# Performance work log

Hardware: AMD Instinct MI355X
Metric: run time of the kernel (lower is better)

Reference implementation:

```python
import jax, jax.numpy as jnp
import numpy as np

NUM_HEADS = 8
QK_CH = 1024
V_CH = 1024
Q_DIM = 1024
KV_DIM = 1024
EPS = 1e-5


def layernorm(x, w, b):
    mu = jnp.mean(x, axis=-1, keepdims=True)
    var = jnp.mean(jnp.square(x - mu), axis=-1, keepdims=True)
    return (x - mu) * jax.lax.rsqrt(var + EPS) * w + b


def setup_inputs() -> dict:
    key = jax.random.key(0)
    ks = jax.random.split(key, 8)
    B, Q, K = 8, 512, 4096
    s = 0.02
    return {
        "hidden_states": jax.random.normal(ks[0], (B, Q, Q_DIM), jnp.float32),
        "inputs": jax.random.normal(ks[1], (B, K, KV_DIM), jnp.float32),
        "ln1_w": jnp.ones((Q_DIM,), jnp.float32),
        "ln1_b": jnp.zeros((Q_DIM,), jnp.float32),
        "ln2_w": jnp.ones((KV_DIM,), jnp.float32),
        "ln2_b": jnp.zeros((KV_DIM,), jnp.float32),
        "Wq": jax.random.normal(ks[2], (QK_CH, Q_DIM), jnp.float32) * s,
        "bq": jnp.zeros((QK_CH,), jnp.float32),
        "Wk": jax.random.normal(ks[3], (QK_CH, KV_DIM), jnp.float32) * s,
        "bk": jnp.zeros((QK_CH,), jnp.float32),
        "Wv": jax.random.normal(ks[4], (V_CH, KV_DIM), jnp.float32) * s,
        "bv": jnp.zeros((V_CH,), jnp.float32),
    }


def reference(hidden_states, inputs, ln1_w, ln1_b, ln2_w, ln2_b, Wq, bq, Wk, bk, Wv, bv):
    B, Qlen, _ = hidden_states.shape
    Klen = inputs.shape[1]
    H = NUM_HEADS
    dqk = QK_CH // H
    dv = V_CH // H

    h = layernorm(hidden_states, ln1_w, ln1_b)
    x = layernorm(inputs, ln2_w, ln2_b)

    # torch Linear: y = x W^T + b
    q = (h @ Wq.T + bq).reshape(B, Qlen, H, dqk).transpose(0, 2, 1, 3)  # b h q d
    k = (x @ Wk.T + bk).reshape(B, Klen, H, dqk).transpose(0, 2, 1, 3)  # b h k d
    v = (x @ Wv.T + bv).reshape(B, Klen, H, dv).transpose(0, 2, 1, 3)   # b h k d

    scores = jnp.einsum("bhqd,bhkd->bhqk", q, k) / jnp.sqrt(jnp.float32(dqk))
    probs = jax.nn.softmax(scores, axis=-1)
    ctx = jnp.einsum("bhqk,bhkd->bhqd", probs, v)
    ctx = ctx.transpose(0, 2, 1, 3).reshape(B, Qlen, H * dv)

    # use_query_residual=True
    return hidden_states + ctx
```

## Files before the change

kernel.cpp:

```cpp
#include <hip/hip_runtime.h>
#include <hip/hip_fp8.h>

typedef __attribute__((ext_vector_type(8))) short short8;
typedef __attribute__((ext_vector_type(4))) short bf16x4;
typedef __attribute__((ext_vector_type(4))) float f32x4;
typedef __attribute__((ext_vector_type(2))) long i64x2;

#define DEV __device__ __forceinline__

DEV unsigned short f2bf(float f) {
    unsigned int u = __builtin_bit_cast(unsigned int, f);
    u += 0x7fffu + ((u >> 16) & 1u);
    return (unsigned short)(u >> 16);
}

DEV unsigned char f2fp8(float f) {
    return __hip_fp8_e4m3(f).__x;
}

#define GLOAD16(gp, lp)                                                        \
    __builtin_amdgcn_global_load_lds(                                          \
        (const __attribute__((address_space(1))) void*)(gp),                   \
        (__attribute__((address_space(3))) void*)(lp), 16, 0, 0)

__global__ __launch_bounds__(256) void prep(
    const float* __restrict__ hidden, const float* __restrict__ inputs,
    const float* __restrict__ ln1w, const float* __restrict__ ln1b,
    const float* __restrict__ ln2w, const float* __restrict__ ln2b,
    const float* __restrict__ Wq, const float* __restrict__ Wk, const float* __restrict__ Wv,
    unsigned char* __restrict__ LNh8, unsigned char* __restrict__ LNx8,
    unsigned char* __restrict__ Wq8, unsigned char* __restrict__ Wk8, unsigned char* __restrict__ Wv8)
{
    if (blockIdx.x < 9216) {
        int row = blockIdx.x * 4 + (threadIdx.x >> 6);
        int lane = threadIdx.x & 63;
        const float *src, *wp, *bp; unsigned char* dst;
        if (row < 4096) { src = hidden + (size_t)row * 1024; wp = ln1w; bp = ln1b; dst = LNh8 + (size_t)row * 1024; }
        else { int r = row - 4096; src = inputs + (size_t)r * 1024; wp = ln2w; bp = ln2b; dst = LNx8 + (size_t)r * 1024; }

        f32x4 v[4];
        float s = 0.f, ss = 0.f;
#pragma unroll
        for (int i = 0; i < 4; ++i) {
            v[i] = *reinterpret_cast<const f32x4*>(src + lane * 16 + i * 4);
#pragma unroll
            for (int j = 0; j < 4; ++j) { s += v[i][j]; ss += v[i][j] * v[i][j]; }
        }
#pragma unroll
        for (int off = 32; off >= 1; off >>= 1) { s += __shfl_xor(s, off); ss += __shfl_xor(ss, off); }
        float mu = s * (1.f / 1024.f);
        float var = fmaxf(ss * (1.f / 1024.f) - mu * mu, 0.f);
        float rs = rsqrtf(var + 1e-5f);

        unsigned char by[16];
#pragma unroll
        for (int i = 0; i < 4; ++i) {
            f32x4 wv = *reinterpret_cast<const f32x4*>(wp + lane * 16 + i * 4);
            f32x4 bv = *reinterpret_cast<const f32x4*>(bp + lane * 16 + i * 4);
#pragma unroll
            for (int j = 0; j < 4; ++j)
                by[i * 4 + j] = f2fp8((v[i][j] - mu) * rs * wv[j] + bv[j]);
        }
        int o = (lane * 16) & 63;
        int s0 = (o < 32) ? 2 * o : 2 * (o - 32) + 8;
        unsigned char* base = dst + (lane >> 2) * 64;
        *reinterpret_cast<unsigned long long*>(base + s0)      = *reinterpret_cast<unsigned long long*>(&by[0]);
        *reinterpret_cast<unsigned long long*>(base + s0 + 16) = *reinterpret_cast<unsigned long long*>(&by[8]);
    } else {
        unsigned tid = (blockIdx.x - 9216) * 256 + threadIdx.x;
        int arr = tid >> 16;
        unsigned idx = tid & 65535u;
        const float* s = (arr == 0) ? Wq : (arr == 1) ? Wk : Wv;
        unsigned char* d = (arr == 0) ? Wq8 : (arr == 1) ? Wk8 : Wv8;
        unsigned char by[16];
#pragma unroll
        for (int i = 0; i < 4; ++i) {
            f32x4 a = *reinterpret_cast<const f32x4*>(s + (size_t)idx * 16 + i * 4);
#pragma unroll
            for (int j = 0; j < 4; ++j) by[i * 4 + j] = f2fp8(a[j] * 64.f);
        }
        int o = (idx & 3) * 16;
        int s0 = (o < 32) ? 2 * o : 2 * (o - 32) + 8;
        unsigned char* base = d + (size_t)(idx >> 2) * 64;
        *reinterpret_cast<unsigned long long*>(base + s0)      = *reinterpret_cast<unsigned long long*>(&by[0]);
        *reinterpret_cast<unsigned long long*>(base + s0 + 16) = *reinterpret_cast<unsigned long long*>(&by[8]);
    }
}

__global__ __launch_bounds__(512, 2) void gemm256(
    const unsigned char* __restrict__ A8, const unsigned char* __restrict__ Ah8,
    const unsigned char* __restrict__ W8, const unsigned char* __restrict__ Wq8,
    const float* __restrict__ bk, const float* __restrict__ bv, const float* __restrict__ bq,
    unsigned short* __restrict__ Cn, unsigned short* __restrict__ Vt, unsigned short* __restrict__ Qm)
{
    __shared__ __align__(16) char smemc[65536];

    int t = threadIdx.x, lane = t & 63, w = t >> 6, g = lane >> 4, lr = lane & 15;
    int wr = w >> 2, wcn = w & 3;
    int R0 = wr * 128, C0 = wcn * 64;

    int id = blockIdx.x;
    int m0, n0, trans = 0;
    const unsigned char *Ab_, *Wb_;
    const float* bias;
    unsigned short* Cout;
    if (id < 1024) {
        int xcd = id & 7, ord = id >> 3;
        int mt = xcd * 16 + ord / 8;
        int nt = ord % 8;
        m0 = mt * 256; n0 = nt * 256;
        Ab_ = A8; Wb_ = W8;
        if (nt < 4) { bias = bk; Cout = Cn; }
        else        { bias = bv; Cout = Vt; trans = 1; }
    } else {
        int id2 = id - 1024;
        int mt = id2 & 15, nt = id2 >> 4;
        m0 = mt * 256; n0 = nt * 256;
        Ab_ = Ah8; Wb_ = Wq8;
        bias = bq; Cout = Qm;
    }

    const unsigned char* Ap = Ab_ + (size_t)m0 * 1024;
    const unsigned char* Wp = Wb_ + (size_t)n0 * 1024;

    f32x4 acc[8][4];
#pragma unroll
    for (int i = 0; i < 8; ++i)
#pragma unroll
        for (int j = 0; j < 4; ++j) acc[i][j] = (f32x4)0.f;

    int schunk = (t & 3) ^ ((t >> 3) & 3);
    auto STAGE1 = [&](int slot, int kt, int q) {
        const unsigned char* P = (q < 2) ? Ap : Wp;
        char* ldsb = smemc + ((q < 2) ? 0 : 32768) + slot * 16384 + (q & 1) * 8192;
        int r = (q & 1) * 128 + (t >> 2);
        const char* gp = (const char*)(P + (size_t)r * 1024 + kt * 64 + schunk * 16);
        GLOAD16(gp, ldsb + (t >> 2) * 64 + (t & 3) * 16);
    };

    STAGE1(0, 0, 0); STAGE1(0, 0, 1); STAGE1(0, 0, 2); STAGE1(0, 0, 3);
    asm volatile("s_waitcnt vmcnt(0)" ::: "memory");
    __builtin_amdgcn_s_barrier();

    int xr = (lr >> 1) & 3;
    int slA = (g ^ xr) * 16;

    for (int kt = 0; kt < 16; ++kt) {
        const int cs = kt & 1;
        const char* Ab = smemc + cs * 16384;
        const char* Bb = smemc + 32768 + cs * 16384;
#pragma unroll
        for (int mq = 0; mq < 2; ++mq) {
            i64x2 af[4], bf[4];
#pragma unroll
            for (int a = 0; a < 4; ++a) {
                int r = R0 + mq * 64 + a * 16 + lr;
                af[a] = *reinterpret_cast<const i64x2*>(Ab + r * 64 + slA);
            }
#pragma unroll
            for (int ni = 0; ni < 4; ++ni) {
                int r = C0 + ni * 16 + lr;
                bf[ni] = *reinterpret_cast<const i64x2*>(Bb + r * 64 + slA);
            }
            if (kt < 15) { STAGE1(cs ^ 1, kt + 1, mq * 2); STAGE1(cs ^ 1, kt + 1, mq * 2 + 1); }
            __builtin_amdgcn_sched_barrier(0);
            __builtin_amdgcn_s_barrier();
            asm volatile("s_waitcnt lgkmcnt(0)" ::: "memory");
            __builtin_amdgcn_sched_barrier(0);
            __builtin_amdgcn_s_setprio(1);
#pragma unroll
            for (int a = 0; a < 4; ++a)
#pragma unroll
                for (int ni = 0; ni < 4; ++ni) {
                    acc[mq * 4 + a][ni] = __builtin_amdgcn_mfma_f32_16x16x32_fp8_fp8(
                        af[a][0], bf[ni][0], acc[mq * 4 + a][ni], 0, 0, 0);
                    acc[mq * 4 + a][ni] = __builtin_amdgcn_mfma_f32_16x16x32_fp8_fp8(
                        af[a][1], bf[ni][1], acc[mq * 4 + a][ni], 0, 0, 0);
                }
            __builtin_amdgcn_s_setprio(0);
            if (mq == 1) asm volatile("s_waitcnt vmcnt(0)" ::: "memory");
            __builtin_amdgcn_sched_barrier(0);
            __builtin_amdgcn_s_barrier();
        }
    }
    __syncthreads();

    const float SC = 0.015625f;
    unsigned short* CtS = (unsigned short*)smemc;
    if (!trans) {
#pragma unroll
        for (int ch = 0; ch < 4; ++ch) {
            if (ch) __syncthreads();
            if (wr == (ch >> 1)) {
                int ma = (ch & 1) * 4;
#pragma unroll
                for (int ni = 0; ni < 4; ++ni) {
                    int c = C0 + ni * 16 + lr;
                    float bvv = bias[n0 + c];
#pragma unroll
                    for (int a = 0; a < 4; ++a)
#pragma unroll
                        for (int j = 0; j < 4; ++j)
                            CtS[(a * 16 + g * 4 + j) * 272 + c] = f2bf(acc[ma + a][ni][j] * SC + bvv);
                }
            }
            __syncthreads();
#pragma unroll
            for (int it = 0; it < 4; ++it) {
                int u2 = it * 512 + t;
                int row = u2 >> 5, c16 = u2 & 31;
                *reinterpret_cast<short8*>(Cout + (size_t)(m0 + ch * 64 + row) * 1024 + n0 + c16 * 8) =
                    *reinterpret_cast<const short8*>(&CtS[row * 272 + c16 * 8]);
            }
        }
    } else {
        int nt = n0 >> 8;
        int hbase = (nt - 4) * 2;
        int b = m0 >> 12, kv0 = m0 & 4095;
#pragma unroll
        for (int ch = 0; ch < 4; ++ch) {
            if (ch) __syncthreads();
            if (wcn == ch) {
#pragma unroll
                for (int ni = 0; ni < 4; ++ni) {
                    int dl = ni * 16 + lr;
                    float bvv = bias[(nt - 4) * 256 + ch * 64 + dl];
#pragma unroll
                    for (int mi = 0; mi < 8; ++mi)
#pragma unroll
                        for (int j = 0; j < 4; ++j)
                            CtS[dl * 272 + R0 + mi * 16 + g * 4 + j] = f2bf(acc[mi][ni][j] * SC + bvv);
                }
            }
            __syncthreads();
            int hh = hbase + (ch >> 1), dbase = (ch & 1) * 64;
            unsigned short* dst = Cout + ((size_t)(b * 8 + hh) * 128 + dbase) * 4096 + kv0;
#pragma unroll
            for (int it = 0; it < 4; ++it) {
                int u2 = it * 512 + t;
                int row = u2 >> 5, c8 = u2 & 31;
                *reinterpret_cast<short8*>(dst + (size_t)row * 4096 + c8 * 8) =
                    *reinterpret_cast<const short8*>(&CtS[row * 272 + c8 * 8]);
            }
        }
    }
}

__global__ __launch_bounds__(256, 2) void attn_kernel(
    const unsigned short* __restrict__ Qm, const unsigned short* __restrict__ Km,
    const unsigned short* __restrict__ VtG, const float* __restrict__ hidden,
    float* __restrict__ out)
{
    __shared__ __align__(16) unsigned short Kl[2][64 * 128];
    __shared__ __align__(16) unsigned short Vt[2][128 * 64];
    __shared__ __align__(16) unsigned short Pl[64 * 64];

    int t = threadIdx.x, lane = t & 63, w = t >> 6, g = lane >> 4, lr = lane & 15;
    int id = blockIdx.x;
    int swz = (id & 7) * 64 + (id >> 3);
    int qt = swz & 7, h = (swz >> 3) & 7, b = swz >> 6;

    short8 qf[4];
#pragma unroll
    for (int kk = 0; kk < 4; ++kk)
        qf[kk] = *reinterpret_cast<const short8*>(
            Qm + (size_t)(b * 512 + qt * 64 + w * 16 + lr) * 1024 + h * 128 + kk * 32 + g * 8);
    asm volatile("s_waitcnt vmcnt(0)" ::: "memory");

    float m2 = 0.f;
    float l = 0.f;
    f32x4 oacc[8];
#pragma unroll
    for (int nf = 0; nf < 8; ++nf) oacc[nf] = (f32x4)0.f;

    const float SCALE = 0.08838834764831845f;
    const float LOG2E = 1.4426950408889634f;
    const float K1 = SCALE * LOG2E;
    const float THR2 = 11.5f;

    size_t kbase = (size_t)b * 4096 * 1024 + h * 128;
    size_t vbase = ((size_t)(b * 8 + h)) * 128 * 4096;

    auto STAGE_K = [&](int buf, int c) {
        int kv0 = c * 64;
#pragma unroll
        for (int i = 0; i < 4; ++i) {
            int rb = w * 16 + i * 4;
            int row = rb + (lane >> 4);
            int cb = ((lane & 15) * 16) ^ ((row & 7) << 4);
            const char* gp = (const char*)(Km + kbase + (size_t)(kv0 + row) * 1024) + cb;
            GLOAD16(gp, &Kl[buf][rb * 128]);
        }
    };
    auto STAGE_V = [&](int buf, int c) {
        int kv0 = c * 64;
#pragma unroll
        for (int i = 0; i < 4; ++i) {
            int db = w * 32 + i * 8;
            int d = db + (lane >> 3);
            int cb = ((lane & 7) * 16) ^ ((d & 7) << 4);
            const char* gp = (const char*)(VtG + vbase + (size_t)d * 4096 + kv0) + cb;
            GLOAD16(gp, &Vt[buf][db * 64]);
        }
    };

    STAGE_K(0, 0); STAGE_V(0, 0);

    for (int c = 0; c < 64; ++c) {
        int cur = c & 1;
        asm volatile("s_waitcnt vmcnt(0) lgkmcnt(0)" ::: "memory");
        __builtin_amdgcn_sched_barrier(0);
        __builtin_amdgcn_s_barrier();
        if (c < 63) { STAGE_K(cur ^ 1, c + 1); STAGE_V(cur ^ 1, c + 1); }

        f32x4 sacc[4];
#pragma unroll
        for (int nf = 0; nf < 4; ++nf) sacc[nf] = (f32x4)0.f;
#pragma unroll
        for (int kk = 0; kk < 4; ++kk) {
            int cb0 = kk * 64 + g * 16;
            short8 kf[4];
#pragma unroll
            for (int nf = 0; nf < 4; ++nf) {
                int row = nf * 16 + lr;
                kf[nf] = *reinterpret_cast<const short8*>(
                    (const char*)&Kl[cur][0] + row * 256 + (cb0 ^ ((row & 7) << 4)));
            }
            __builtin_amdgcn_s_setprio(1);
#pragma unroll
            for (int nf = 0; nf < 4; ++nf)
                sacc[nf] = __builtin_amdgcn_mfma_f32_16x16x32_bf16(kf[nf], qf[kk], sacc[nf], 0, 0, 0);
            __builtin_amdgcn_s_setprio(0);
        }

        float smax = sacc[0][0];
#pragma unroll
        for (int nf = 0; nf < 4; ++nf)
#pragma unroll
            for (int j = 0; j < 4; ++j) smax = fmaxf(smax, sacc[nf][j]);
        float s2max = smax * K1;
        if (!__all(s2max <= m2 + THR2)) {
            float rm = s2max;
            rm = fmaxf(rm, __shfl_xor(rm, 16));
            rm = fmaxf(rm, __shfl_xor(rm, 32));
            float m2n = fmaxf(m2, rm);
            float corr = exp2f(m2 - m2n);
            l *= corr;
            m2 = m2n;
#pragma unroll
            for (int j = 0; j < 4; ++j) {
                float cj = __shfl(corr, g * 4 + j);
#pragma unroll
                for (int nf = 0; nf < 8; ++nf) oacc[nf][j] *= cj;
            }
        }
        int prow = w * 16 + lr;
        int rsw = (lr & 7) << 4;
#pragma unroll
        for (int nf = 0; nf < 4; ++nf) {
            float p0 = exp2f(sacc[nf][0] * K1 - m2);
            float p1 = exp2f(sacc[nf][1] * K1 - m2);
            float p2 = exp2f(sacc[nf][2] * K1 - m2);
            float p3 = exp2f(sacc[nf][3] * K1 - m2);
            l += (p0 + p1) + (p2 + p3);
            bf16x4 pk;
            pk[0] = (short)f2bf(p0); pk[1] = (short)f2bf(p1);
            pk[2] = (short)f2bf(p2); pk[3] = (short)f2bf(p3);
            *reinterpret_cast<bf16x4*>(
                (char*)Pl + prow * 128 + ((nf * 32 + g * 8) ^ rsw)) = pk;
        }
        asm volatile("s_waitcnt lgkmcnt(0)" ::: "memory");
        __builtin_amdgcn_sched_barrier(0);

#pragma unroll
        for (int kp = 0; kp < 2; ++kp) {
            int cb0 = kp * 64 + g * 16;
            short8 pa = *reinterpret_cast<const short8*>(
                (const char*)Pl + prow * 128 + (cb0 ^ rsw));
#pragma unroll
            for (int nf = 0; nf < 8; ++nf) {
                int d = nf * 16 + lr;
                short8 vb = *reinterpret_cast<const short8*>(
                    (const char*)&Vt[cur][0] + d * 128 + (cb0 ^ ((d & 7) << 4)));
                oacc[nf] = __builtin_amdgcn_mfma_f32_16x16x32_bf16(pa, vb, oacc[nf], 0, 0, 0);
            }
        }
    }

    l += __shfl_xor(l, 16);
    l += __shfl_xor(l, 32);
#pragma unroll
    for (int j = 0; j < 4; ++j) {
        float lj = __shfl(l, g * 4 + j);
        float inv = 1.f / lj;
        int q = qt * 64 + w * 16 + g * 4 + j;
        size_t base = (size_t)(b * 512 + q) * 1024 + h * 128;
#pragma unroll
        for (int nf = 0; nf < 8; ++nf) {
            int d = nf * 16 + lr;
            out[base + d] = hidden[base + d] + oacc[nf][j] * inv;
        }
    }
}

extern "C" void kernel_launch(void* const* d_in, const int* in_sizes, int n_in,
                              void* d_out, int out_size, void* d_ws, size_t ws_size,
                              hipStream_t stream) {
    const float* hidden = (const float*)d_in[0];
    const float* inputs = (const float*)d_in[1];
    const float* ln1w   = (const float*)d_in[2];
    const float* ln1b   = (const float*)d_in[3];
    const float* ln2w   = (const float*)d_in[4];
    const float* ln2b   = (const float*)d_in[5];
    const float* Wq     = (const float*)d_in[6];
    const float* bq     = (const float*)d_in[7];
    const float* Wk     = (const float*)d_in[8];
    const float* bk     = (const float*)d_in[9];
    const float* Wv     = (const float*)d_in[10];
    const float* bv     = (const float*)d_in[11];
    float* out = (float*)d_out;
    char* ws = (char*)d_ws;

    unsigned char* LNh8 = (unsigned char*)ws;
    unsigned char* LNx8 = LNh8 + 4194304;
    unsigned char* Wq8  = LNx8 + 33554432;
    unsigned char* Wk8  = Wq8 + 1048576;
    unsigned char* Wv8  = Wk8 + 1048576;
    unsigned short* Qm  = (unsigned short*)(Wv8 + 1048576);
    unsigned short* Km  = Qm + 4194304;
    unsigned short* VtG = Km + 33554432;

    prep<<<dim3(9984), dim3(256), 0, stream>>>(
        hidden, inputs, ln1w, ln1b, ln2w, ln2b, Wq, Wk, Wv, LNh8, LNx8, Wq8, Wk8, Wv8);
    gemm256<<<dim3(1088), dim3(512), 0, stream>>>(
        LNx8, LNh8, Wk8, Wq8, bk, bv, bq, Km, VtG, Qm);
    attn_kernel<<<dim3(512), dim3(256), 0, stream>>>(Qm, Km, VtG, hidden, out);
}
```

Measured before the change: 298.4 us.

## Give each attention wave two query tiles and reuse B fragments in GEMM

The attention kernel now runs two waves per block instead of four, and each wave handles 32 query rows as two 16-row sub-tiles. Each K and V fragment read from LDS then feeds twice as many MFMAs, cutting shared-memory traffic per unit of math. This costs more registers, fewer waves to hide latency, and more staging loads per thread, and launch bounds drop to a minimum of one block. The GEMM main loop is also unrolled by hand so the B fragments loaded in the first half are reused in the second half instead of being reloaded.

```diff
diff --git a/kernel.cpp b/kernel.cpp
--- a/kernel.cpp
+++ b/kernel.cpp
@@ -149,39 +149,61 @@
         const int cs = kt & 1;
         const char* Ab = smemc + cs * 16384;
         const char* Bb = smemc + 32768 + cs * 16384;
-#pragma unroll
-        for (int mq = 0; mq < 2; ++mq) {
-            i64x2 af[4], bf[4];
-#pragma unroll
-            for (int a = 0; a < 4; ++a) {
-                int r = R0 + mq * 64 + a * 16 + lr;
-                af[a] = *reinterpret_cast<const i64x2*>(Ab + r * 64 + slA);
-            }
+        i64x2 af[4], bf[4];
+
+#pragma unroll
+        for (int a = 0; a < 4; ++a) {
+            int r = R0 + a * 16 + lr;
+            af[a] = *reinterpret_cast<const i64x2*>(Ab + r * 64 + slA);
+        }
+#pragma unroll
+        for (int ni = 0; ni < 4; ++ni) {
+            int r = C0 + ni * 16 + lr;
+            bf[ni] = *reinterpret_cast<const i64x2*>(Bb + r * 64 + slA);
+        }
+        if (kt < 15) { STAGE1(cs ^ 1, kt + 1, 0); STAGE1(cs ^ 1, kt + 1, 1); }
+        __builtin_amdgcn_sched_barrier(0);
+        __builtin_amdgcn_s_barrier();
+        asm volatile("s_waitcnt lgkmcnt(0)" ::: "memory");
+        __builtin_amdgcn_sched_barrier(0);
+        __builtin_amdgcn_s_setprio(1);
+#pragma unroll
+        for (int a = 0; a < 4; ++a)
 #pragma unroll
             for (int ni = 0; ni < 4; ++ni) {
-                int r = C0 + ni * 16 + lr;
-                bf[ni] = *reinterpret_cast<const i64x2*>(Bb + r * 64 + slA);
-            }
-            if (kt < 15) { STAGE1(cs ^ 1, kt + 1, mq * 2); STAGE1(cs ^ 1, kt + 1, mq * 2 + 1); }
-            __builtin_amdgcn_sched_barrier(0);
-            __builtin_amdgcn_s_barrier();
-            asm volatile("s_waitcnt lgkmcnt(0)" ::: "memory");
-            __builtin_amdgcn_sched_barrier(0);
-            __builtin_amdgcn_s_setprio(1);
-#pragma unroll
-            for (int a = 0; a < 4; ++a)
-#pragma unroll
-                for (int ni = 0; ni < 4; ++ni) {
-                    acc[mq * 4 + a][ni] = __builtin_amdgcn_mfma_f32_16x16x32_fp8_fp8(
-                        af[a][0], bf[ni][0], acc[mq * 4 + a][ni], 0, 0, 0);
-                    acc[mq * 4 + a][ni] = __builtin_amdgcn_mfma_f32_16x16x32_fp8_fp8(
-                        af[a][1], bf[ni][1], acc[mq * 4 + a][ni], 0, 0, 0);
-                }
-            __builtin_amdgcn_s_setprio(0);
-            if (mq == 1) asm volatile("s_waitcnt vmcnt(0)" ::: "memory");
-            __builtin_amdgcn_sched_barrier(0);
-            __builtin_amdgcn_s_barrier();
-        }
+                acc[a][ni] = __builtin_amdgcn_mfma_f32_16x16x32_fp8_fp8(
+                    af[a][0], bf[ni][0], acc[a][ni], 0, 0, 0);
+                acc[a][ni] = __builtin_amdgcn_mfma_f32_16x16x32_fp8_fp8(
+                    af[a][1], bf[ni][1], acc[a][ni], 0, 0, 0);
+            }
+        __builtin_amdgcn_s_setprio(0);
+        __builtin_amdgcn_sched_barrier(0);
+        __builtin_amdgcn_s_barrier();
+
+#pragma unroll
+        for (int a = 0; a < 4; ++a) {
+            int r = R0 + 64 + a * 16 + lr;
+            af[a] = *reinterpret_cast<const i64x2*>(Ab + r * 64 + slA);
+        }
+        if (kt < 15) { STAGE1(cs ^ 1, kt + 1, 2); STAGE1(cs ^ 1, kt + 1, 3); }
+        __builtin_amdgcn_sched_barrier(0);
+        __builtin_amdgcn_s_barrier();
+        asm volatile("s_waitcnt lgkmcnt(0)" ::: "memory");
+        __builtin_amdgcn_sched_barrier(0);
+        __builtin_amdgcn_s_setprio(1);
+#pragma unroll
+        for (int a = 0; a < 4; ++a)
+#pragma unroll
+            for (int ni = 0; ni < 4; ++ni) {
+                acc[4 + a][ni] = __builtin_amdgcn_mfma_f32_16x16x32_fp8_fp8(
+                    af[a][0], bf[ni][0], acc[4 + a][ni], 0, 0, 0);
+                acc[4 + a][ni] = __builtin_amdgcn_mfma_f32_16x16x32_fp8_fp8(
+                    af[a][1], bf[ni][1], acc[4 + a][ni], 0, 0, 0);
+            }
+        __builtin_amdgcn_s_setprio(0);
+        asm volatile("s_waitcnt vmcnt(0)" ::: "memory");
+        __builtin_amdgcn_sched_barrier(0);
+        __builtin_amdgcn_s_barrier();
     }
     __syncthreads();
 
@@ -246,7 +268,7 @@
     }
 }
 
-__global__ __launch_bounds__(256, 2) void attn_kernel(
+__global__ __launch_bounds__(128, 1) void attn_kernel(
     const unsigned short* __restrict__ Qm, const unsigned short* __restrict__ Km,
     const unsigned short* __restrict__ VtG, const float* __restrict__ hidden,
     float* __restrict__ out)
@@ -260,18 +282,22 @@
     int swz = (id & 7) * 64 + (id >> 3);
     int qt = swz & 7, h = (swz >> 3) & 7, b = swz >> 6;
 
-    short8 qf[4];
-#pragma unroll
-    for (int kk = 0; kk < 4; ++kk)
-        qf[kk] = *reinterpret_cast<const short8*>(
-            Qm + (size_t)(b * 512 + qt * 64 + w * 16 + lr) * 1024 + h * 128 + kk * 32 + g * 8);
+    short8 qf[2][4];
+#pragma unroll
+    for (int mi = 0; mi < 2; ++mi)
+#pragma unroll
+        for (int kk = 0; kk < 4; ++kk)
+            qf[mi][kk] = *reinterpret_cast<const short8*>(
+                Qm + (size_t)(b * 512 + qt * 64 + w * 32 + mi * 16 + lr) * 1024 + h * 128 + kk * 32 + g * 8);
     asm volatile("s_waitcnt vmcnt(0)" ::: "memory");
 
-    float m2 = 0.f;
-    float l = 0.f;
-    f32x4 oacc[8];
-#pragma unroll
-    for (int nf = 0; nf < 8; ++nf) oacc[nf] = (f32x4)0.f;
+    float m2[2] = {0.f, 0.f};
+    float lsum[2] = {0.f, 0.f};
+    f32x4 oacc[2][8];
+#pragma unroll
+    for (int mi = 0; mi < 2; ++mi)
+#pragma unroll
+        for (int nf = 0; nf < 8; ++nf) oacc[mi][nf] = (f32x4)0.f;
 
     const float SCALE = 0.08838834764831845f;
     const float LOG2E = 1.4426950408889634f;
@@ -284,8 +310,8 @@
     auto STAGE_K = [&](int buf, int c) {
         int kv0 = c * 64;
 #pragma unroll
-        for (int i = 0; i < 4; ++i) {
-            int rb = w * 16 + i * 4;
+        for (int i = 0; i < 8; ++i) {
+            int rb = w * 32 + i * 4;
             int row = rb + (lane >> 4);
             int cb = ((lane & 15) * 16) ^ ((row & 7) << 4);
             const char* gp = (const char*)(Km + kbase + (size_t)(kv0 + row) * 1024) + cb;
@@ -295,8 +321,8 @@
     auto STAGE_V = [&](int buf, int c) {
         int kv0 = c * 64;
 #pragma unroll
-        for (int i = 0; i < 4; ++i) {
-            int db = w * 32 + i * 8;
+        for (int i = 0; i < 8; ++i) {
+            int db = w * 64 + i * 8;
             int d = db + (lane >> 3);
             int cb = ((lane & 7) * 16) ^ ((d & 7) << 4);
             const char* gp = (const char*)(VtG + vbase + (size_t)d * 4096 + kv0) + cb;
@@ -306,6 +332,8 @@
 
     STAGE_K(0, 0); STAGE_V(0, 0);
 
+    int rsw = (lr & 7) << 4;
+
     for (int c = 0; c < 64; ++c) {
         int cur = c & 1;
         asm volatile("s_waitcnt vmcnt(0) lgkmcnt(0)" ::: "memory");
@@ -313,9 +341,11 @@
         __builtin_amdgcn_s_barrier();
         if (c < 63) { STAGE_K(cur ^ 1, c + 1); STAGE_V(cur ^ 1, c + 1); }
 
-        f32x4 sacc[4];
-#pragma unroll
-        for (int nf = 0; nf < 4; ++nf) sacc[nf] = (f32x4)0.f;
+        f32x4 sacc[2][4];
+#pragma unroll
+        for (int mi = 0; mi < 2; ++mi)
+#pragma unroll
+            for (int nf = 0; nf < 4; ++nf) sacc[mi][nf] = (f32x4)0.f;
 #pragma unroll
         for (int kk = 0; kk < 4; ++kk) {
             int cb0 = kk * 64 + g * 16;
@@ -328,46 +358,50 @@
             }
             __builtin_amdgcn_s_setprio(1);
 #pragma unroll
+            for (int mi = 0; mi < 2; ++mi)
+#pragma unroll
+                for (int nf = 0; nf < 4; ++nf)
+                    sacc[mi][nf] = __builtin_amdgcn_mfma_f32_16x16x32_bf16(kf[nf], qf[mi][kk], sacc[mi][nf], 0, 0, 0);
+            __builtin_amdgcn_s_setprio(0);
+        }
+
+#pragma unroll
+        for (int mi = 0; mi < 2; ++mi) {
+            float smax = sacc[mi][0][0];
+#pragma unroll
             for (int nf = 0; nf < 4; ++nf)
-                sacc[nf] = __builtin_amdgcn_mfma_f32_16x16x32_bf16(kf[nf], qf[kk], sacc[nf], 0, 0, 0);
-            __builtin_amdgcn_s_setprio(0);
-        }
-
-        float smax = sacc[0][0];
-#pragma unroll
-        for (int nf = 0; nf < 4; ++nf)
-#pragma unroll
-            for (int j = 0; j < 4; ++j) smax = fmaxf(smax, sacc[nf][j]);
-        float s2max = smax * K1;
-        if (!__all(s2max <= m2 + THR2)) {
-            float rm = s2max;
-            rm = fmaxf(rm, __shfl_xor(rm, 16));
-            rm = fmaxf(rm, __shfl_xor(rm, 32));
-            float m2n = fmaxf(m2, rm);
-            float corr = exp2f(m2 - m2n);
-            l *= corr;
-            m2 = m2n;
-#pragma unroll
-            for (int j = 0; j < 4; ++j) {
-                float cj = __shfl(corr, g * 4 + j);
-#pragma unroll
-                for (int nf = 0; nf < 8; ++nf) oacc[nf][j] *= cj;
-            }
-        }
-        int prow = w * 16 + lr;
-        int rsw = (lr & 7) << 4;
-#pragma unroll
-        for (int nf = 0; nf < 4; ++nf) {
-            float p0 = exp2f(sacc[nf][0] * K1 - m2);
-            float p1 = exp2f(sacc[nf][1] * K1 - m2);
-            float p2 = exp2f(sacc[nf][2] * K1 - m2);
-            float p3 = exp2f(sacc[nf][3] * K1 - m2);
-            l += (p0 + p1) + (p2 + p3);
-            bf16x4 pk;
-            pk[0] = (short)f2bf(p0); pk[1] = (short)f2bf(p1);
-            pk[2] = (short)f2bf(p2); pk[3] = (short)f2bf(p3);
-            *reinterpret_cast<bf16x4*>(
-                (char*)Pl + prow * 128 + ((nf * 32 + g * 8) ^ rsw)) = pk;
+#pragma unroll
+                for (int j = 0; j < 4; ++j) smax = fmaxf(smax, sacc[mi][nf][j]);
+            float s2max = smax * K1;
+            if (!__all(s2max <= m2[mi] + THR2)) {
+                float rm = s2max;
+                rm = fmaxf(rm, __shfl_xor(rm, 16));
+                rm = fmaxf(rm, __shfl_xor(rm, 32));
+                float m2n = fmaxf(m2[mi], rm);
+                float corr = exp2f(m2[mi] - m2n);
+                lsum[mi] *= corr;
+                m2[mi] = m2n;
+#pragma unroll
+                for (int j = 0; j < 4; ++j) {
+                    float cj = __shfl(corr, g * 4 + j);
+#pragma unroll
+                    for (int nf = 0; nf < 8; ++nf) oacc[mi][nf][j] *= cj;
+                }
+            }
+            int prow = w * 32 + mi * 16 + lr;
+#pragma unroll
+            for (int nf = 0; nf < 4; ++nf) {
+                float p0 = exp2f(sacc[mi][nf][0] * K1 - m2[mi]);
+                float p1 = exp2f(sacc[mi][nf][1] * K1 - m2[mi]);
+                float p2 = exp2f(sacc[mi][nf][2] * K1 - m2[mi]);
+                float p3 = exp2f(sacc[mi][nf][3] * K1 - m2[mi]);
+                lsum[mi] += (p0 + p1) + (p2 + p3);
+                bf16x4 pk;
+                pk[0] = (short)f2bf(p0); pk[1] = (short)f2bf(p1);
+                pk[2] = (short)f2bf(p2); pk[3] = (short)f2bf(p3);
+                *reinterpret_cast<bf16x4*>(
+                    (char*)Pl + prow * 128 + ((nf * 32 + g * 8) ^ rsw)) = pk;
+            }
         }
         asm volatile("s_waitcnt lgkmcnt(0)" ::: "memory");
         __builtin_amdgcn_sched_barrier(0);
@@ -375,30 +409,41 @@
 #pragma unroll
         for (int kp = 0; kp < 2; ++kp) {
             int cb0 = kp * 64 + g * 16;
-            short8 pa = *reinterpret_cast<const short8*>(
-                (const char*)Pl + prow * 128 + (cb0 ^ rsw));
+            short8 pa[2];
+#pragma unroll
+            for (int mi = 0; mi < 2; ++mi) {
+                int prow = w * 32 + mi * 16 + lr;
+                pa[mi] = *reinterpret_cast<const short8*>(
+                    (const char*)Pl + prow * 128 + (cb0 ^ rsw));
+            }
 #pragma unroll
             for (int nf = 0; nf < 8; ++nf) {
                 int d = nf * 16 + lr;
                 short8 vb = *reinterpret_cast<const short8*>(
                     (const char*)&Vt[cur][0] + d * 128 + (cb0 ^ ((d & 7) << 4)));
-                oacc[nf] = __builtin_amdgcn_mfma_f32_16x16x32_bf16(pa, vb, oacc[nf], 0, 0, 0);
-            }
-        }
-    }
-
-    l += __shfl_xor(l, 16);
-    l += __shfl_xor(l, 32);
-#pragma unroll
-    for (int j = 0; j < 4; ++j) {
-        float lj = __shfl(l, g * 4 + j);
-        float inv = 1.f / lj;
-        int q = qt * 64 + w * 16 + g * 4 + j;
-        size_t base = (size_t)(b * 512 + q) * 1024 + h * 128;
-#pragma unroll
-        for (int nf = 0; nf < 8; ++nf) {
-            int d = nf * 16 + lr;
-            out[base + d] = hidden[base + d] + oacc[nf][j] * inv;
+#pragma unroll
+                for (int mi = 0; mi < 2; ++mi)
+                    oacc[mi][nf] = __builtin_amdgcn_mfma_f32_16x16x32_bf16(pa[mi], vb, oacc[mi][nf], 0, 0, 0);
+            }
+        }
+    }
+
+#pragma unroll
+    for (int mi = 0; mi < 2; ++mi) {
+        float lv = lsum[mi];
+        lv += __shfl_xor(lv, 16);
+        lv += __shfl_xor(lv, 32);
+#pragma unroll
+        for (int j = 0; j < 4; ++j) {
+            float lj = __shfl(lv, g * 4 + j);
+            float inv = 1.f / lj;
+            int q = qt * 64 + w * 32 + mi * 16 + g * 4 + j;
+            size_t base = (size_t)(b * 512 + q) * 1024 + h * 128;
+#pragma unroll
+            for (int nf = 0; nf < 8; ++nf) {
+                int d = nf * 16 + lr;
+                out[base + d] = hidden[base + d] + oacc[mi][nf][j] * inv;
+            }
         }
     }
 }
@@ -434,5 +479,5 @@
         hidden, inputs, ln1w, ln1b, ln2w, ln2b, Wq, Wk, Wv, LNh8, LNx8, Wq8, Wk8, Wv8);
     gemm256<<<dim3(1088), dim3(512), 0, stream>>>(
         LNx8, LNh8, Wk8, Wq8, bk, bv, bq, Km, VtG, Qm);
-    attn_kernel<<<dim3(512), dim3(256), 0, stream>>>(Qm, Km, VtG, hidden, out);
-}
+    attn_kernel<<<dim3(512), dim3(128), 0, stream>>>(Qm, Km, VtG, hidden, out);
+}
```

Measured after the change: 339.5 us. +13.8%, slower.
